# Kernel optimization log

Measured on AMD Instinct MI355X. Metric: run time of the kernel, lower is better.

The kernel has to match this reference:

```python
import jax, jax.numpy as jnp
import numpy as np

N_MODELS = 64
IN_F = 256
OUT_F = 256
BATCH = 8192


def setup_inputs() -> dict:
    key = jax.random.key(0)
    kx, kw, kb, ki = jax.random.split(key, 4)
    x = jax.random.normal(kx, (BATCH, OUT_F), dtype=jnp.float32)
    idxs = jax.random.randint(ki, (BATCH,), 0, N_MODELS, dtype=jnp.int64)
    # learned parameters (torch inits them to zeros; we use random so grads/outputs are nontrivial)
    w = jax.random.normal(kw, (N_MODELS, IN_F, OUT_F), dtype=jnp.float32) * 0.02
    b = jax.random.normal(kb, (N_MODELS, OUT_F), dtype=jnp.float32) * 0.02
    return {"x": x, "idxs": idxs, "w": w, "b": b}


def reference(x, idxs, w, b):
    # torch: baddbmm(b[idxs,:,None], w[idxs], x[:,:,None]).squeeze(-1) -> relu
    # y[n, i] = b[idxs[n], i] + sum_o w[idxs[n], i, o] * x[n, o]
    wg = w[idxs]                      # (B, in, out) gathered per-sample weights
    bg = b[idxs]                      # (B, out)
    y = jnp.einsum('bio,bo->bi', wg, x) + bg
    return jax.nn.relu(y)
```

## Files before the change

### kernel.cpp

```cpp
#include <hip/hip_runtime.h>
#include <stdint.h>


#define N_MODELS 64
#define IN_F     256
#define OUT_F    256
#define BATCH    8192
#define BM       128
#define BN       128
#define PK       264

typedef __bf16 bf16x8 __attribute__((ext_vector_type(8)));
typedef float  f32x4  __attribute__((ext_vector_type(4)));

__device__ __forceinline__ bf16x8 pack8(float4 a, float4 b) {
  bf16x8 o;
  o[0] = (__bf16)a.x; o[1] = (__bf16)a.y; o[2] = (__bf16)a.z; o[3] = (__bf16)a.w;
  o[4] = (__bf16)b.x; o[5] = (__bf16)b.y; o[6] = (__bf16)b.z; o[7] = (__bf16)b.w;
  return o;
}

__global__ __launch_bounds__(1024) void fused_kernel(
    const float* __restrict__ x, const int* __restrict__ idxs,
    const float* __restrict__ w, const float* __restrict__ bias_g,
    float* __restrict__ out) {
  const int bid   = blockIdx.x;
  const int model = ((bid >> 4) << 2) | ((bid >> 1) & 3);
  const int tile  = (bid >> 3) & 1;
  const int i0    = (bid & 1) * BN;
  const int t     = threadIdx.x;
  const int lane  = t & 63;
  const int wv    = t >> 6;

  __shared__ unsigned short a_lds[BM][PK];
  __shared__ unsigned short b_lds[BN][PK];
  __shared__ int rid[BM];
  __shared__ int wsum[16];

  const int rw = t >> 3;
  const int h  = t & 7;

  const int4* ip = (const int4*)idxs + t * 2;
  int4 iv0 = ip[0], iv1 = ip[1];

  const float* wrow = w + (size_t)model * (IN_F * OUT_F)
                        + (size_t)(i0 + rw) * IN_F + h * 32;
  {
    float4 tw[8];
#pragma unroll
    for (int j = 0; j < 8; ++j) tw[j] = *(const float4*)(wrow + j * 4);
#pragma unroll
    for (int j = 0; j < 4; ++j)
      *(bf16x8*)&b_lds[rw][h * 32 + j * 8] = pack8(tw[2 * j], tw[2 * j + 1]);
  }

  if (t < BM) rid[t] = -1;

  int cnt = (iv0.x == model) + (iv0.y == model) + (iv0.z == model) + (iv0.w == model)
          + (iv1.x == model) + (iv1.y == model) + (iv1.z == model) + (iv1.w == model);
  int inc = cnt;
#pragma unroll
  for (int d = 1; d < 64; d <<= 1) {
    int u = __shfl_up(inc, d);
    if (lane >= d) inc += u;
  }
  if (lane == 63) wsum[wv] = inc;
  __syncthreads();
  int wpre = 0, total = 0;
#pragma unroll
  for (int j = 0; j < 16; ++j) {
    int s = wsum[j];
    total += s;
    if (j < wv) wpre += s;
  }
  const int start = tile * BM;
  if (start >= total) return;
  int off = wpre + inc - cnt - start;
  {
    int n0 = t * 8;
    if (iv0.x == model) { if ((unsigned)off < BM) rid[off] = n0 + 0; ++off; }
    if (iv0.y == model) { if ((unsigned)off < BM) rid[off] = n0 + 1; ++off; }
    if (iv0.z == model) { if ((unsigned)off < BM) rid[off] = n0 + 2; ++off; }
    if (iv0.w == model) { if ((unsigned)off < BM) rid[off] = n0 + 3; ++off; }
    if (iv1.x == model) { if ((unsigned)off < BM) rid[off] = n0 + 4; ++off; }
    if (iv1.y == model) { if ((unsigned)off < BM) rid[off] = n0 + 5; ++off; }
    if (iv1.z == model) { if ((unsigned)off < BM) rid[off] = n0 + 6; ++off; }
    if (iv1.w == model) { if ((unsigned)off < BM) rid[off] = n0 + 7; ++off; }
  }
  __syncthreads();

  const int srow = rid[rw];
  const float* xrow = x + (size_t)(srow < 0 ? 0 : srow) * IN_F + h * 32;
  {
    float4 tx[8];
#pragma unroll
    for (int j = 0; j < 8; ++j) tx[j] = *(const float4*)(xrow + j * 4);
#pragma unroll
    for (int j = 0; j < 4; ++j)
      *(bf16x8*)&a_lds[rw][h * 32 + j * 8] = pack8(tx[2 * j], tx[2 * j + 1]);
  }

  const int wm   = (wv & 3) * 32;
  const int wn   = (wv >> 2) * 32;
  const int col  = lane & 15;
  const int quad = lane >> 4;
  float bv[2];
  const float* bp = bias_g + model * OUT_F + i0 + wn + col;
#pragma unroll
  for (int nt = 0; nt < 2; ++nt) bv[nt] = bp[nt * 16];

  __syncthreads();

  f32x4 acc[2][2];
#pragma unroll
  for (int mt = 0; mt < 2; ++mt)
#pragma unroll
    for (int nt = 0; nt < 2; ++nt)
      acc[mt][nt] = (f32x4){bv[nt], bv[nt], bv[nt], bv[nt]};

#pragma unroll
  for (int ks = 0; ks < 8; ++ks) {
    bf16x8 af[2], bfr[2];
#pragma unroll
    for (int mt = 0; mt < 2; ++mt)
      af[mt] = *(const bf16x8*)&a_lds[wm + mt * 16 + col][ks * 32 + quad * 8];
#pragma unroll
    for (int nt = 0; nt < 2; ++nt)
      bfr[nt] = *(const bf16x8*)&b_lds[wn + nt * 16 + col][ks * 32 + quad * 8];
#pragma unroll
    for (int mt = 0; mt < 2; ++mt)
#pragma unroll
      for (int nt = 0; nt < 2; ++nt)
        acc[mt][nt] = __builtin_amdgcn_mfma_f32_16x16x32_bf16(
            af[mt], bfr[nt], acc[mt][nt], 0, 0, 0);
  }

#pragma unroll
  for (int mt = 0; mt < 2; ++mt) {
#pragma unroll
    for (int reg = 0; reg < 4; ++reg) {
      const int mm = wm + mt * 16 + quad * 4 + reg;
      const int s = rid[mm];
      if (s >= 0) {
        float* orow = out + (size_t)s * OUT_F + i0 + wn + col;
#pragma unroll
        for (int nt = 0; nt < 2; ++nt)
          orow[nt * 16] = fmaxf(acc[mt][nt][reg], 0.0f);
      }
    }
  }
}

extern "C" void kernel_launch(void* const* d_in, const int* in_sizes, int n_in,
                              void* d_out, int out_size, void* d_ws, size_t ws_size,
                              hipStream_t stream) {
  const float* x    = (const float*)d_in[0];
  const int*   idxs = (const int*)d_in[1];
  const float* w    = (const float*)d_in[2];
  const float* b    = (const float*)d_in[3];
  float* out = (float*)d_out;
  (void)d_ws; (void)ws_size;

  fused_kernel<<<N_MODELS * 4, 1024, 0, stream>>>(x, idxs, w, b, out);
}
```

Baseline: 86.39 us.

## Drop LDS staging and feed MFMA directly from global loads with smaller blocks

Removes the shared-memory staging of the x rows and weight tiles. Each wave now loads its MFMA fragments straight from global memory as float4 pairs and converts them to bf16 in registers. Blocks shrink to 512 threads covering a 128x64 output tile, so the grid grows to 512 blocks, and the block-to-model mapping is rearranged. This cuts the LDS footprint and two barriers and should raise occupancy, but the fragment loads are strided per lane (about 32 bytes per row) and poorly coalesced. Each row of x is also re-read by several waves, leaning on the L2 cache.

```diff
diff --git a/kernel.cpp b/kernel.cpp
--- a/kernel.cpp
+++ b/kernel.cpp
@@ -5,128 +5,115 @@
 #define N_MODELS 64
 #define IN_F     256
 #define OUT_F    256
-#define BATCH    8192
 #define BM       128
-#define BN       128
-#define PK       264
 
 typedef __bf16 bf16x8 __attribute__((ext_vector_type(8)));
 typedef float  f32x4  __attribute__((ext_vector_type(4)));
 
-__device__ __forceinline__ bf16x8 pack8(float4 a, float4 b) {
+__device__ __forceinline__ bf16x8 cvt8(float4 a, float4 b) {
   bf16x8 o;
   o[0] = (__bf16)a.x; o[1] = (__bf16)a.y; o[2] = (__bf16)a.z; o[3] = (__bf16)a.w;
   o[4] = (__bf16)b.x; o[5] = (__bf16)b.y; o[6] = (__bf16)b.z; o[7] = (__bf16)b.w;
   return o;
 }
 
-__global__ __launch_bounds__(1024) void fused_kernel(
+__global__ __launch_bounds__(512) void fused_kernel(
     const float* __restrict__ x, const int* __restrict__ idxs,
     const float* __restrict__ w, const float* __restrict__ bias_g,
     float* __restrict__ out) {
   const int bid   = blockIdx.x;
-  const int model = ((bid >> 4) << 2) | ((bid >> 1) & 3);
-  const int tile  = (bid >> 3) & 1;
-  const int i0    = (bid & 1) * BN;
+  const int model = (bid & 7) | ((bid >> 6) << 3);
+  const int i0    = ((bid >> 3) & 3) * 64;
+  const int tile  = (bid >> 5) & 1;
   const int t     = threadIdx.x;
   const int lane  = t & 63;
   const int wv    = t >> 6;
 
-  __shared__ unsigned short a_lds[BM][PK];
-  __shared__ unsigned short b_lds[BN][PK];
   __shared__ int rid[BM];
-  __shared__ int wsum[16];
+  __shared__ int wsum[8];
 
-  const int rw = t >> 3;
-  const int h  = t & 7;
+  const int wm   = (wv & 3) * 32;
+  const int wn   = (wv >> 2) * 32;
+  const int col  = lane & 15;
+  const int quad = lane >> 4;
 
-  const int4* ip = (const int4*)idxs + t * 2;
-  int4 iv0 = ip[0], iv1 = ip[1];
+  const float* bp = bias_g + model * OUT_F + i0 + wn + col;
+  const float bv0 = bp[0];
+  const float bv1 = bp[16];
 
-  const float* wrow = w + (size_t)model * (IN_F * OUT_F)
-                        + (size_t)(i0 + rw) * IN_F + h * 32;
-  {
-    float4 tw[8];
+  if (t < BM) rid[t] = 0;
+
+  const int4* ip = (const int4*)idxs + t * 4;
+  int4 iv[4];
 #pragma unroll
-    for (int j = 0; j < 8; ++j) tw[j] = *(const float4*)(wrow + j * 4);
+  for (int j = 0; j < 4; ++j) iv[j] = ip[j];
+  int cnt = 0;
 #pragma unroll
-    for (int j = 0; j < 4; ++j)
-      *(bf16x8*)&b_lds[rw][h * 32 + j * 8] = pack8(tw[2 * j], tw[2 * j + 1]);
+  for (int j = 0; j < 4; ++j) {
+    int4 v = iv[j];
+    cnt += (v.x == model) + (v.y == model) + (v.z == model) + (v.w == model);
   }
-
-  if (t < BM) rid[t] = -1;
-
-  int cnt = (iv0.x == model) + (iv0.y == model) + (iv0.z == model) + (iv0.w == model)
-          + (iv1.x == model) + (iv1.y == model) + (iv1.z == model) + (iv1.w == model);
   int inc = cnt;
 #pragma unroll
   for (int d = 1; d < 64; d <<= 1) {
-    int u = __shfl_up(inc, d);
-    if (lane >= d) inc += u;
+    int s = __shfl_up(inc, d);
+    if (lane >= d) inc += s;
   }
   if (lane == 63) wsum[wv] = inc;
   __syncthreads();
   int wpre = 0, total = 0;
 #pragma unroll
-  for (int j = 0; j < 16; ++j) {
+  for (int j = 0; j < 8; ++j) {
     int s = wsum[j];
     total += s;
     if (j < wv) wpre += s;
   }
   const int start = tile * BM;
-  if (start >= total) return;
   int off = wpre + inc - cnt - start;
-  {
-    int n0 = t * 8;
-    if (iv0.x == model) { if ((unsigned)off < BM) rid[off] = n0 + 0; ++off; }
-    if (iv0.y == model) { if ((unsigned)off < BM) rid[off] = n0 + 1; ++off; }
-    if (iv0.z == model) { if ((unsigned)off < BM) rid[off] = n0 + 2; ++off; }
-    if (iv0.w == model) { if ((unsigned)off < BM) rid[off] = n0 + 3; ++off; }
-    if (iv1.x == model) { if ((unsigned)off < BM) rid[off] = n0 + 4; ++off; }
-    if (iv1.y == model) { if ((unsigned)off < BM) rid[off] = n0 + 5; ++off; }
-    if (iv1.z == model) { if ((unsigned)off < BM) rid[off] = n0 + 6; ++off; }
-    if (iv1.w == model) { if ((unsigned)off < BM) rid[off] = n0 + 7; ++off; }
+#pragma unroll
+  for (int j = 0; j < 4; ++j) {
+    int4 v = iv[j];
+    int n0 = t * 16 + j * 4;
+    if (v.x == model) { if ((unsigned)off < BM) rid[off] = n0 + 0; ++off; }
+    if (v.y == model) { if ((unsigned)off < BM) rid[off] = n0 + 1; ++off; }
+    if (v.z == model) { if ((unsigned)off < BM) rid[off] = n0 + 2; ++off; }
+    if (v.w == model) { if ((unsigned)off < BM) rid[off] = n0 + 3; ++off; }
   }
   __syncthreads();
+  if (start >= total) return;
+  const int rows = min(total - start, BM);
 
-  const int srow = rid[rw];
-  const float* xrow = x + (size_t)(srow < 0 ? 0 : srow) * IN_F + h * 32;
-  {
-    float4 tx[8];
+  const float* pA[2];
 #pragma unroll
-    for (int j = 0; j < 8; ++j) tx[j] = *(const float4*)(xrow + j * 4);
+  for (int mt = 0; mt < 2; ++mt)
+    pA[mt] = x + (size_t)rid[wm + mt * 16 + col] * IN_F + quad * 8;
+  const float* pB[2];
 #pragma unroll
-    for (int j = 0; j < 4; ++j)
-      *(bf16x8*)&a_lds[rw][h * 32 + j * 8] = pack8(tx[2 * j], tx[2 * j + 1]);
-  }
-
-  const int wm   = (wv & 3) * 32;
-  const int wn   = (wv >> 2) * 32;
-  const int col  = lane & 15;
-  const int quad = lane >> 4;
-  float bv[2];
-  const float* bp = bias_g + model * OUT_F + i0 + wn + col;
-#pragma unroll
-  for (int nt = 0; nt < 2; ++nt) bv[nt] = bp[nt * 16];
-
-  __syncthreads();
+  for (int nt = 0; nt < 2; ++nt)
+    pB[nt] = w + (size_t)model * (IN_F * OUT_F)
+               + (size_t)(i0 + wn + nt * 16 + col) * IN_F + quad * 8;
 
   f32x4 acc[2][2];
-#pragma unroll
-  for (int mt = 0; mt < 2; ++mt)
-#pragma unroll
-    for (int nt = 0; nt < 2; ++nt)
-      acc[mt][nt] = (f32x4){bv[nt], bv[nt], bv[nt], bv[nt]};
+  acc[0][0] = (f32x4){bv0, bv0, bv0, bv0};
+  acc[1][0] = acc[0][0];
+  acc[0][1] = (f32x4){bv1, bv1, bv1, bv1};
+  acc[1][1] = acc[0][1];
 
 #pragma unroll
   for (int ks = 0; ks < 8; ++ks) {
     bf16x8 af[2], bfr[2];
 #pragma unroll
-    for (int mt = 0; mt < 2; ++mt)
-      af[mt] = *(const bf16x8*)&a_lds[wm + mt * 16 + col][ks * 32 + quad * 8];
+    for (int mt = 0; mt < 2; ++mt) {
+      float4 a0 = *(const float4*)(pA[mt] + ks * 32);
+      float4 a1 = *(const float4*)(pA[mt] + ks * 32 + 4);
+      af[mt] = cvt8(a0, a1);
+    }
 #pragma unroll
-    for (int nt = 0; nt < 2; ++nt)
-      bfr[nt] = *(const bf16x8*)&b_lds[wn + nt * 16 + col][ks * 32 + quad * 8];
+    for (int nt = 0; nt < 2; ++nt) {
+      float4 b0 = *(const float4*)(pB[nt] + ks * 32);
+      float4 b1 = *(const float4*)(pB[nt] + ks * 32 + 4);
+      bfr[nt] = cvt8(b0, b1);
+    }
 #pragma unroll
     for (int mt = 0; mt < 2; ++mt)
 #pragma unroll
@@ -140,12 +127,11 @@
 #pragma unroll
     for (int reg = 0; reg < 4; ++reg) {
       const int mm = wm + mt * 16 + quad * 4 + reg;
-      const int s = rid[mm];
-      if (s >= 0) {
+      if (mm < rows) {
+        const int s = rid[mm];
         float* orow = out + (size_t)s * OUT_F + i0 + wn + col;
-#pragma unroll
-        for (int nt = 0; nt < 2; ++nt)
-          orow[nt * 16] = fmaxf(acc[mt][nt][reg], 0.0f);
+        orow[0]  = fmaxf(acc[mt][0][reg], 0.0f);
+        orow[16] = fmaxf(acc[mt][1][reg], 0.0f);
       }
     }
   }
@@ -161,5 +147,5 @@
   float* out = (float*)d_out;
   (void)d_ws; (void)ws_size;
 
-  fused_kernel<<<N_MODELS * 4, 1024, 0, stream>>>(x, idxs, w, b, out);
+  fused_kernel<<<512, 512, 0, stream>>>(x, idxs, w, b, out);
 }
```

Measured after the change: 103.4 us. 1.2x slower.
